# Optimization experiments

Hardware: AMD Instinct MI355X
Metric: run time of the kernel (lower is better)

Reference implementation:

```python
import jax, jax.numpy as jnp
import numpy as np
from jax import lax

T = 8192
OBS = 512
HID = 2048
NOBJ = 8


def setup_inputs() -> dict:
    key = jax.random.key(0)
    ks = jax.random.split(key, 9)
    s_in = 1.0 / np.sqrt(OBS)
    s_hid = 1.0 / np.sqrt(HID)
    return {
        "x": jax.random.normal(ks[0], (T, OBS), dtype=jnp.float32),
        "W_in": jax.random.normal(ks[1], (HID, OBS), dtype=jnp.float32) * s_in,
        "W_B": jax.random.normal(ks[2], (HID, OBS), dtype=jnp.float32) * s_in,
        "W_C": jax.random.normal(ks[3], (HID, OBS), dtype=jnp.float32) * s_in,
        "W_delta": jax.random.normal(ks[4], (HID, OBS), dtype=jnp.float32) * s_in,
        "A_log": jax.random.normal(ks[5], (HID,), dtype=jnp.float32),
        "W_out": jax.random.normal(ks[6], (NOBJ, HID), dtype=jnp.float32) * s_hid,
        "b_out": jnp.zeros((NOBJ,), dtype=jnp.float32),
        "W_skip": jax.random.normal(ks[7], (NOBJ, OBS), dtype=jnp.float32) * s_in,
    }


def reference(x, W_in, W_B, W_C, W_delta, A_log, W_out, b_out, W_skip):
    # Input-dependent SSM parameters (4 GEMMs, [T, HID] each)
    x_state = x @ W_in.T
    B = x @ W_B.T
    C = x @ W_C.T
    delta = jax.nn.sigmoid(x @ W_delta.T)
    A = -jnp.exp(A_log)                      # [HID]

    A_bar = jnp.exp(delta * A)               # [T, HID], per-step decay
    Bx = B * x_state                         # [T, HID], per-step input

    def step(h, inp):
        a, bx = inp
        h = a * h + bx
        return h, h

    h0 = jnp.zeros((HID,), dtype=x.dtype)
    _, h_seq = lax.scan(step, h0, (A_bar, Bx))  # [T, HID]

    y = C * h_seq
    out = y @ W_out.T + b_out + x @ W_skip.T    # [T, NOBJ]
    return out
```

## Files before the change

### kernel.cpp

```cpp
#include <hip/hip_runtime.h>
#include <hip/hip_bf16.h>
#include <cstdint>

#define TT   8192
#define KOBS 512
#define HID  2048
#define NOBJ 8
#define NCH  64
#define CT   128

typedef unsigned short u16;
typedef uint32_t u32;
typedef short bf16x8 __attribute__((ext_vector_type(8)));
typedef float f32x4  __attribute__((ext_vector_type(4)));
typedef unsigned short u16x4 __attribute__((ext_vector_type(4)));

static __device__ __forceinline__ float bf2f(u16 u) {
    union { uint32_t i; float f; } v;
    v.i = ((uint32_t)u) << 16;
    return v.f;
}
static __device__ __forceinline__ u16 f2bf(float f) {
    union { float f; uint32_t i; } v;
    v.f = f;
    uint32_t lsb = (v.i >> 16) & 1u;
    uint32_t r = v.i + 0x7fffu + lsb;
    return (u16)(r >> 16);
}

static __device__ __forceinline__ void async_ld16(const u16* g, u16* l) {
    __builtin_amdgcn_global_load_lds(
        (const __attribute__((address_space(1))) uint32_t*)g,
        (__attribute__((address_space(3))) uint32_t*)l,
        16, 0, 0);
}

__global__ void prep_w(const float* __restrict__ Win,
                       const float* __restrict__ WB,
                       const float* __restrict__ WC,
                       const float* __restrict__ Wd,
                       const float* __restrict__ A_log,
                       u16* __restrict__ W_bf,
                       float* __restrict__ A_e)
{
    const int tid0   = blockIdx.x * blockDim.x + threadIdx.x;
    const int stride = gridDim.x * blockDim.x;

    for (int i = tid0; i < 4 * HID * KOBS / 8; i += stride) {
        int n  = i >> 6;
        int k8 = (i & 63) * 8;
        int h  = n >> 2;
        int w  = n & 3;
        const float* src = (w == 0) ? Win : (w == 1) ? WB : (w == 2) ? WC : Wd;
        const float4* s4 = (const float4*)(src + (size_t)h * KOBS + k8);
        float4 a = s4[0], b = s4[1];
        u16x4 o1 = { f2bf(a.x), f2bf(a.y), f2bf(a.z), f2bf(a.w) };
        u16x4 o2 = { f2bf(b.x), f2bf(b.y), f2bf(b.z), f2bf(b.w) };
        *(u16x4*)&W_bf[(size_t)i * 8]     = o1;
        *(u16x4*)&W_bf[(size_t)i * 8 + 4] = o2;
    }

    if (tid0 < HID)
        A_e[tid0] = -__expf(A_log[tid0]) * 1.44269504f;
}

__launch_bounds__(256)
__global__ void prep_x_out(const float* __restrict__ x,
                           const float* __restrict__ b_out,
                           const float* __restrict__ W_skip,
                           float* __restrict__ out,
                           u16* __restrict__ x_bf)
{
    const int wave = threadIdx.x >> 6;
    const int lane = threadIdx.x & 63;
    const int t0 = (blockIdx.x * 4 + wave) * 4;

    float acc[4][NOBJ];
#pragma unroll
    for (int tt = 0; tt < 4; tt++)
#pragma unroll
        for (int o = 0; o < NOBJ; o++) acc[tt][o] = 0.f;

#pragma unroll
    for (int i = 0; i < 2; i++) {
        const int kv = (i * 64 + lane) * 4;
        float4 w[NOBJ];
#pragma unroll
        for (int o = 0; o < NOBJ; o++)
            w[o] = *(const float4*)(W_skip + (size_t)o * KOBS + kv);
#pragma unroll
        for (int tt = 0; tt < 4; tt++) {
            const size_t off = (size_t)(t0 + tt) * KOBS + kv;
            float4 xv = *(const float4*)(x + off);
            u16x4 xb = { f2bf(xv.x), f2bf(xv.y), f2bf(xv.z), f2bf(xv.w) };
            *(u16x4*)&x_bf[off] = xb;
#pragma unroll
            for (int o = 0; o < NOBJ; o++)
                acc[tt][o] += xv.x * w[o].x + xv.y * w[o].y +
                              xv.z * w[o].z + xv.w * w[o].w;
        }
    }
#pragma unroll
    for (int s = 32; s > 0; s >>= 1)
#pragma unroll
        for (int tt = 0; tt < 4; tt++)
#pragma unroll
            for (int o = 0; o < NOBJ; o++)
                acc[tt][o] += __shfl_xor(acc[tt][o], s, 64);
    if (lane == 0) {
#pragma unroll
        for (int tt = 0; tt < 4; tt++)
#pragma unroll
            for (int o = 0; o < NOBJ; o++)
                out[(size_t)(t0 + tt) * NOBJ + o] = acc[tt][o] + b_out[o];
    }
}

__launch_bounds__(256)
__global__ void gemm_fused(const u16* __restrict__ x_bf,
                           const u16* __restrict__ W_bf,
                           const float* __restrict__ A_e,
                           u16* __restrict__ YB,
                           u16* __restrict__ YC,
                           float* __restrict__ P,
                           float* __restrict__ S)
{
    __shared__ __align__(16) u16 smem[3 * 128 * 40];
    __shared__ float Ps[256], Ss[256];
    u16* a_s = smem;
    u16* b_s = smem + 4096;

    const int tid  = threadIdx.x;
    const int bm   = blockIdx.x & 63;
    const int bn   = blockIdx.x >> 6;
    const int m0t  = bm * 128;
    const int n0   = bn * 128;
    const int lane = tid & 63;
    const int wave = tid >> 6;
    const int wn   = (wave & 1) * 64;
    const int wt   = (wave >> 1) * 64;
    const int fr   = lane & 15;
    const int fq   = lane >> 4;

    f32x4 acc[4][4];
#pragma unroll
    for (int i = 0; i < 4; i++)
#pragma unroll
        for (int j = 0; j < 4; j++) {
            f32x4 z = {0.f, 0.f, 0.f, 0.f};
            acc[i][j] = z;
        }

    const int srow = tid >> 2;
    const int scg  = (tid & 3) ^ ((srow >> 1) & 3);
    const u16* gA0 = x_bf + (size_t)(m0t + srow) * KOBS + scg * 8;
    const u16* gA1 = gA0 + (size_t)64 * KOBS;
    const u16* gB0 = W_bf + (size_t)(n0 + srow) * KOBS + scg * 8;
    const u16* gB1 = gB0 + (size_t)64 * KOBS;
    u16* lA0 = &a_s[tid * 8];
    u16* lA1 = &a_s[2048 + tid * 8];
    u16* lB0 = &b_s[tid * 8];
    u16* lB1 = &b_s[2048 + tid * 8];

    const int pcg = fq ^ ((fr >> 1) & 3);

    for (int kb = 0; kb < KOBS; kb += 32) {
        async_ld16(gA0 + kb, lA0);
        async_ld16(gA1 + kb, lA1);
        async_ld16(gB0 + kb, lB0);
        async_ld16(gB1 + kb, lB1);
        __syncthreads();

        bf16x8 af[4], bfx[4];
#pragma unroll
        for (int i = 0; i < 4; i++)
            af[i] = *(const bf16x8*)&b_s[(wn + i * 16 + fr) * 32 + pcg * 8];
#pragma unroll
        for (int j = 0; j < 4; j++)
            bfx[j] = *(const bf16x8*)&a_s[(wt + j * 16 + fr) * 32 + pcg * 8];

#pragma unroll
        for (int i = 0; i < 4; i++)
#pragma unroll
            for (int j = 0; j < 4; j++)
                acc[i][j] = __builtin_amdgcn_mfma_f32_16x16x32_bf16(
                    af[i], bfx[j], acc[i][j], 0, 0, 0);
        __syncthreads();
    }

    const int hq = wn >> 2;
#pragma unroll
    for (int i = 0; i < 4; i++) {
        const int hl = hq + i * 4 + fq;
        const float ae = A_e[bn * 32 + hl];
#pragma unroll
        for (int j = 0; j < 4; j++) {
            const int tl = wt + j * 16 + fr;
            f32x4 v = acc[i][j];
            float sig = 1.0f / (1.0f + __expf(-v[3]));
            smem[(0 * 128 + tl) * 40 + hl] = f2bf(v[0] * v[1]);
            smem[(1 * 128 + tl) * 40 + hl] = f2bf(v[2]);
            smem[(2 * 128 + tl) * 40 + hl] = f2bf(sig * ae);
        }
    }
    __syncthreads();

    const int hi  = tid & 31;
    const int seg = tid >> 5;
    {
        float p = 1.f, s = 0.f;
        const int tbase = seg * 16;
#pragma unroll
        for (int t = 0; t < 16; t++) {
            float a  = exp2f(bf2f(smem[(2 * 128 + tbase + t) * 40 + hi]));
            float bx = bf2f(smem[(0 * 128 + tbase + t) * 40 + hi]);
            s = fmaf(a, s, bx);
            p *= a;
        }
        Ps[seg * 32 + hi] = p;
        Ss[seg * 32 + hi] = s;
    }
    __syncthreads();

    if (tid < 32) {
        float rr = 1.f, sr = 0.f;
#pragma unroll
        for (int sg = 0; sg < 8; sg++) {
            float ps = Ps[sg * 32 + tid], ss = Ss[sg * 32 + tid];
            Ps[sg * 32 + tid] = rr;
            Ss[sg * 32 + tid] = sr;
            sr = fmaf(ps, sr, ss);
            rr *= ps;
        }
        P[(size_t)bm * HID + bn * 32 + tid] = rr;
        S[(size_t)bm * HID + bn * 32 + tid] = sr;
    }
    __syncthreads();

    {
        const float Rp = Ps[seg * 32 + hi];
        const float Sp = Ss[seg * 32 + hi];
        float r = 1.f, s = 0.f;
        const int tbase = seg * 16;
#pragma unroll
        for (int t = 0; t < 16; t++) {
            const int row = tbase + t;
            float a  = exp2f(bf2f(smem[(2 * 128 + row) * 40 + hi]));
            float bx = bf2f(smem[(0 * 128 + row) * 40 + hi]);
            float cc = bf2f(smem[(1 * 128 + row) * 40 + hi]);
            s = fmaf(a, s, bx);
            r *= a;
            float hl = fmaf(r, Sp, s);
            smem[(0 * 128 + row) * 40 + hi] = f2bf(cc * hl);
            smem[(2 * 128 + row) * 40 + hi] = f2bf(cc * r * Rp);
        }
    }
    __syncthreads();

#pragma unroll
    for (int it = 0; it < 4; it++) {
        const int g = it * 64 + (tid >> 2);
        const int a = g >> 7;
        const int t = g & 127;
        const int c = tid & 3;
        uint4 vd = *(const uint4*)&smem[((a * 2) * 128 + t) * 40 + c * 8];
        u16* dst = (a == 0 ? YB : YC) +
                   (size_t)(m0t + t) * HID + bn * 32 + c * 8;
        *(uint4*)dst = vd;
    }
}

__global__ void scan_combine(const float* __restrict__ P,
                             const float* __restrict__ S,
                             float* __restrict__ H0)
{
    const int h = blockIdx.x * 256 + threadIdx.x;
    float hrun = 0.f;
#pragma unroll 8
    for (int c = 0; c < NCH; c++) {
        H0[c * HID + h] = hrun;
        hrun = fmaf(P[c * HID + h], hrun, S[c * HID + h]);
    }
}

__launch_bounds__(256)
__global__ void final_out(const u16* __restrict__ YB,
                          const u16* __restrict__ YC,
                          const float* __restrict__ H0,
                          const float* __restrict__ W_out,
                          float* __restrict__ out)
{
    __shared__ __align__(16) u16 ybuf[64 * 256];
    __shared__ __align__(16) u16 wst[8 * 264];
    __shared__ float h0s[256];
    const int tid  = threadIdx.x;
    const int tc   = blockIdx.x >> 3;
    const int hg   = blockIdx.x & 7;
    const int lane = tid & 63;
    const int wave = tid >> 6;
    const int fr   = lane & 15;
    const int fq   = lane >> 4;
    const int t0   = tc * 64;

#pragma unroll
    for (int o = 0; o < 8; o++)
        wst[o * 264 + tid] = f2bf(W_out[(size_t)o * HID + hg * 256 + tid]);
    h0s[tid] = H0[(size_t)(tc >> 1) * HID + hg * 256 + tid];
    __syncthreads();

    const int g   = tid & 31;
    const int tb0 = tid >> 5;
    float4 h0a = *(const float4*)&h0s[g * 8];
    float4 h0b = *(const float4*)&h0s[g * 8 + 4];
    const float h0r[8] = { h0a.x, h0a.y, h0a.z, h0a.w,
                           h0b.x, h0b.y, h0b.z, h0b.w };
#pragma unroll
    for (int k = 0; k < 8; k++) {
        const int t = tb0 + k * 8;
        const size_t off = (size_t)(t0 + t) * HID + hg * 256 + g * 8;
        bf16x8 yb = *(const bf16x8*)(YB + off);
        bf16x8 yc = *(const bf16x8*)(YC + off);
        bf16x8 yv;
#pragma unroll
        for (int e = 0; e < 8; e++) {
            float y = fmaf(bf2f((u16)yc[e]), h0r[e], bf2f((u16)yb[e]));
            yv[e] = (short)f2bf(y);
        }
        *(bf16x8*)&ybuf[t * 256 + ((g ^ (t & 7)) << 3)] = yv;
    }
    __syncthreads();

    bf16x8 bw[8];
#pragma unroll
    for (int ks = 0; ks < 8; ks++) {
        bf16x8 w = {0, 0, 0, 0, 0, 0, 0, 0};
        if (fr < 8)
            w = *(const bf16x8*)&wst[fr * 264 + ks * 32 + fq * 8];
        bw[ks] = w;
    }

    {
        const int t = wave * 16 + fr;
        f32x4 acc2 = {0.f, 0.f, 0.f, 0.f};
#pragma unroll
        for (int ks = 0; ks < 8; ks++) {
            const int gg = ks * 4 + fq;
            bf16x8 yv = *(const bf16x8*)
                &ybuf[t * 256 + ((gg ^ (fr & 7)) << 3)];
            acc2 = __builtin_amdgcn_mfma_f32_16x16x32_bf16(bw[ks], yv, acc2,
                                                           0, 0, 0);
        }
        if (fq < 2) {
            const int tg = t0 + t;
#pragma unroll
            for (int reg = 0; reg < 4; reg++)
                atomicAdd(&out[(size_t)tg * NOBJ + 4 * fq + reg], acc2[reg]);
        }
    }
}

extern "C" void kernel_launch(void* const* d_in, const int* in_sizes, int n_in,
                              void* d_out, int out_size, void* d_ws, size_t ws_size,
                              hipStream_t stream)
{
    const float* x      = (const float*)d_in[0];
    const float* Win    = (const float*)d_in[1];
    const float* WB     = (const float*)d_in[2];
    const float* WC     = (const float*)d_in[3];
    const float* Wd     = (const float*)d_in[4];
    const float* A_log  = (const float*)d_in[5];
    const float* W_out  = (const float*)d_in[6];
    const float* b_out  = (const float*)d_in[7];
    const float* W_skip = (const float*)d_in[8];
    float* out = (float*)d_out;

    char* ws = (char*)d_ws;
    size_t off = 0;
    auto alloc = [&](size_t bytes) -> void* {
        void* p = (void*)(ws + off);
        off += (bytes + 255) & ~(size_t)255;
        return p;
    };

    u16*   x_bf = (u16*)  alloc((size_t)TT * KOBS * 2);
    u16*   W_bf = (u16*)  alloc((size_t)4 * HID * KOBS * 2);
    float* A_e  = (float*)alloc((size_t)HID * 4);
    u16*   YB   = (u16*)  alloc((size_t)TT * HID * 2);
    u16*   YC   = (u16*)  alloc((size_t)TT * HID * 2);
    float* P    = (float*)alloc((size_t)NCH * HID * 4);
    float* S    = (float*)alloc((size_t)NCH * HID * 4);
    float* H0   = (float*)alloc((size_t)NCH * HID * 4);
    (void)ws_size; (void)in_sizes; (void)n_in; (void)out_size;

    prep_w<<<2048, 256, 0, stream>>>(Win, WB, WC, Wd, A_log, W_bf, A_e);
    prep_x_out<<<512, 256, 0, stream>>>(x, b_out, W_skip, out, x_bf);
    gemm_fused<<<4096, 256, 0, stream>>>(x_bf, W_bf, A_e, YB, YC, P, S);
    scan_combine<<<8, 256, 0, stream>>>(P, S, H0);
    final_out<<<1024, 256, 0, stream>>>(YB, YC, H0, W_out, out);
}
```

Measured before the change: 217.3 us.

## Fuse YB output projection into GEMM epilogue and merge prep kernels

The local-scan part of y (C times intra-chunk h) is now projected through W_out with an MFMA inside gemm_fused and atomically added to out, so the YB intermediate is never written to or read from global memory. final_out now only reads YC and folds H0 into scaled W_out weights. The two prep kernels are merged into one launch, and the second in-block scan pass is replaced by a vectorized combine using stored prefix values. The cost is many float atomics on out and bf16 rounding of intermediate prefix states.

```diff
diff --git a/kernel.cpp b/kernel.cpp
--- a/kernel.cpp
+++ b/kernel.cpp
@@ -14,6 +14,7 @@
 typedef short bf16x8 __attribute__((ext_vector_type(8)));
 typedef float f32x4  __attribute__((ext_vector_type(4)));
 typedef unsigned short u16x4 __attribute__((ext_vector_type(4)));
+typedef unsigned short u16x8 __attribute__((ext_vector_type(8)));
 
 static __device__ __forceinline__ float bf2f(u16 u) {
     union { uint32_t i; float f; } v;
@@ -35,84 +36,84 @@
         16, 0, 0);
 }
 
-__global__ void prep_w(const float* __restrict__ Win,
-                       const float* __restrict__ WB,
-                       const float* __restrict__ WC,
-                       const float* __restrict__ Wd,
-                       const float* __restrict__ A_log,
-                       u16* __restrict__ W_bf,
-                       float* __restrict__ A_e)
+__launch_bounds__(256)
+__global__ void prep_all(const float* __restrict__ x,
+                         const float* __restrict__ Win,
+                         const float* __restrict__ WB,
+                         const float* __restrict__ WC,
+                         const float* __restrict__ Wd,
+                         const float* __restrict__ A_log,
+                         const float* __restrict__ b_out,
+                         const float* __restrict__ W_skip,
+                         float* __restrict__ out,
+                         u16* __restrict__ x_bf,
+                         u16* __restrict__ W_bf,
+                         float* __restrict__ A_e)
 {
-    const int tid0   = blockIdx.x * blockDim.x + threadIdx.x;
-    const int stride = gridDim.x * blockDim.x;
-
-    for (int i = tid0; i < 4 * HID * KOBS / 8; i += stride) {
-        int n  = i >> 6;
-        int k8 = (i & 63) * 8;
-        int h  = n >> 2;
-        int w  = n & 3;
-        const float* src = (w == 0) ? Win : (w == 1) ? WB : (w == 2) ? WC : Wd;
-        const float4* s4 = (const float4*)(src + (size_t)h * KOBS + k8);
-        float4 a = s4[0], b = s4[1];
-        u16x4 o1 = { f2bf(a.x), f2bf(a.y), f2bf(a.z), f2bf(a.w) };
-        u16x4 o2 = { f2bf(b.x), f2bf(b.y), f2bf(b.z), f2bf(b.w) };
-        *(u16x4*)&W_bf[(size_t)i * 8]     = o1;
-        *(u16x4*)&W_bf[(size_t)i * 8 + 4] = o2;
-    }
-
-    if (tid0 < HID)
-        A_e[tid0] = -__expf(A_log[tid0]) * 1.44269504f;
-}
-
-__launch_bounds__(256)
-__global__ void prep_x_out(const float* __restrict__ x,
-                           const float* __restrict__ b_out,
-                           const float* __restrict__ W_skip,
-                           float* __restrict__ out,
-                           u16* __restrict__ x_bf)
-{
-    const int wave = threadIdx.x >> 6;
-    const int lane = threadIdx.x & 63;
-    const int t0 = (blockIdx.x * 4 + wave) * 4;
-
-    float acc[4][NOBJ];
-#pragma unroll
-    for (int tt = 0; tt < 4; tt++)
-#pragma unroll
-        for (int o = 0; o < NOBJ; o++) acc[tt][o] = 0.f;
-
-#pragma unroll
-    for (int i = 0; i < 2; i++) {
-        const int kv = (i * 64 + lane) * 4;
-        float4 w[NOBJ];
-#pragma unroll
-        for (int o = 0; o < NOBJ; o++)
-            w[o] = *(const float4*)(W_skip + (size_t)o * KOBS + kv);
-#pragma unroll
-        for (int tt = 0; tt < 4; tt++) {
-            const size_t off = (size_t)(t0 + tt) * KOBS + kv;
-            float4 xv = *(const float4*)(x + off);
-            u16x4 xb = { f2bf(xv.x), f2bf(xv.y), f2bf(xv.z), f2bf(xv.w) };
-            *(u16x4*)&x_bf[off] = xb;
+    if (blockIdx.x < 512) {
+        const int wave = threadIdx.x >> 6;
+        const int lane = threadIdx.x & 63;
+        const int t0 = (blockIdx.x * 4 + wave) * 4;
+
+        float acc[4][NOBJ];
+#pragma unroll
+        for (int tt = 0; tt < 4; tt++)
+#pragma unroll
+            for (int o = 0; o < NOBJ; o++) acc[tt][o] = 0.f;
+
+#pragma unroll
+        for (int i = 0; i < 2; i++) {
+            const int kv = (i * 64 + lane) * 4;
+            float4 w[NOBJ];
 #pragma unroll
             for (int o = 0; o < NOBJ; o++)
-                acc[tt][o] += xv.x * w[o].x + xv.y * w[o].y +
-                              xv.z * w[o].z + xv.w * w[o].w;
-        }
-    }
-#pragma unroll
-    for (int s = 32; s > 0; s >>= 1)
-#pragma unroll
-        for (int tt = 0; tt < 4; tt++)
-#pragma unroll
-            for (int o = 0; o < NOBJ; o++)
-                acc[tt][o] += __shfl_xor(acc[tt][o], s, 64);
-    if (lane == 0) {
-#pragma unroll
-        for (int tt = 0; tt < 4; tt++)
-#pragma unroll
-            for (int o = 0; o < NOBJ; o++)
-                out[(size_t)(t0 + tt) * NOBJ + o] = acc[tt][o] + b_out[o];
+                w[o] = *(const float4*)(W_skip + (size_t)o * KOBS + kv);
+#pragma unroll
+            for (int tt = 0; tt < 4; tt++) {
+                const size_t off = (size_t)(t0 + tt) * KOBS + kv;
+                float4 xv = *(const float4*)(x + off);
+                u16x4 xb = { f2bf(xv.x), f2bf(xv.y), f2bf(xv.z), f2bf(xv.w) };
+                *(u16x4*)&x_bf[off] = xb;
+#pragma unroll
+                for (int o = 0; o < NOBJ; o++)
+                    acc[tt][o] += xv.x * w[o].x + xv.y * w[o].y +
+                                  xv.z * w[o].z + xv.w * w[o].w;
+            }
+        }
+#pragma unroll
+        for (int s = 32; s > 0; s >>= 1)
+#pragma unroll
+            for (int tt = 0; tt < 4; tt++)
+#pragma unroll
+                for (int o = 0; o < NOBJ; o++)
+                    acc[tt][o] += __shfl_xor(acc[tt][o], s, 64);
+        if (lane == 0) {
+#pragma unroll
+            for (int tt = 0; tt < 4; tt++)
+#pragma unroll
+                for (int o = 0; o < NOBJ; o++)
+                    out[(size_t)(t0 + tt) * NOBJ + o] = acc[tt][o] + b_out[o];
+        }
+    } else {
+        const int tid0 = (blockIdx.x - 512) * 256 + threadIdx.x;
+#pragma unroll
+        for (int q = 0; q < 2; q++) {
+            const int i = tid0 + q * 262144;
+            int n  = i >> 6;
+            int k8 = (i & 63) * 8;
+            int h  = n >> 2;
+            int w  = n & 3;
+            const float* src = (w == 0) ? Win : (w == 1) ? WB
+                             : (w == 2) ? WC  : Wd;
+            const float4* s4 = (const float4*)(src + (size_t)h * KOBS + k8);
+            float4 a = s4[0], b = s4[1];
+            u16x4 o1 = { f2bf(a.x), f2bf(a.y), f2bf(a.z), f2bf(a.w) };
+            u16x4 o2 = { f2bf(b.x), f2bf(b.y), f2bf(b.z), f2bf(b.w) };
+            *(u16x4*)&W_bf[(size_t)i * 8]     = o1;
+            *(u16x4*)&W_bf[(size_t)i * 8 + 4] = o2;
+        }
+        if (tid0 < HID)
+            A_e[tid0] = -__expf(A_log[tid0]) * 1.44269504f;
     }
 }
 
@@ -120,10 +121,11 @@
 __global__ void gemm_fused(const u16* __restrict__ x_bf,
                            const u16* __restrict__ W_bf,
                            const float* __restrict__ A_e,
-                           u16* __restrict__ YB,
+                           const float* __restrict__ W_out,
                            u16* __restrict__ YC,
                            float* __restrict__ P,
-                           float* __restrict__ S)
+                           float* __restrict__ S,
+                           float* __restrict__ out)
 {
     __shared__ __align__(16) u16 smem[3 * 128 * 40];
     __shared__ float Ps[256], Ss[256];
@@ -205,17 +207,20 @@
     }
     __syncthreads();
 
-    const int hi  = tid & 31;
-    const int seg = tid >> 5;
     {
+        const int hi  = tid & 31;
+        const int seg = tid >> 5;
         float p = 1.f, s = 0.f;
         const int tbase = seg * 16;
 #pragma unroll
         for (int t = 0; t < 16; t++) {
-            float a  = exp2f(bf2f(smem[(2 * 128 + tbase + t) * 40 + hi]));
-            float bx = bf2f(smem[(0 * 128 + tbase + t) * 40 + hi]);
+            const int row = tbase + t;
+            float a  = exp2f(bf2f(smem[(2 * 128 + row) * 40 + hi]));
+            float bx = bf2f(smem[(0 * 128 + row) * 40 + hi]);
             s = fmaf(a, s, bx);
             p *= a;
+            smem[(0 * 128 + row) * 40 + hi] = f2bf(s);
+            smem[(2 * 128 + row) * 40 + hi] = f2bf(p);
         }
         Ps[seg * 32 + hi] = p;
         Ss[seg * 32 + hi] = s;
@@ -237,36 +242,61 @@
     }
     __syncthreads();
 
-    {
-        const float Rp = Ps[seg * 32 + hi];
-        const float Sp = Ss[seg * 32 + hi];
-        float r = 1.f, s = 0.f;
-        const int tbase = seg * 16;
-#pragma unroll
-        for (int t = 0; t < 16; t++) {
-            const int row = tbase + t;
-            float a  = exp2f(bf2f(smem[(2 * 128 + row) * 40 + hi]));
-            float bx = bf2f(smem[(0 * 128 + row) * 40 + hi]);
-            float cc = bf2f(smem[(1 * 128 + row) * 40 + hi]);
-            s = fmaf(a, s, bx);
-            r *= a;
-            float hl = fmaf(r, Sp, s);
-            smem[(0 * 128 + row) * 40 + hi] = f2bf(cc * hl);
-            smem[(2 * 128 + row) * 40 + hi] = f2bf(cc * r * Rp);
-        }
+#pragma unroll
+    for (int it = 0; it < 2; it++) {
+        const int idx = it * 256 + tid;
+        const int t   = idx >> 2;
+        const int cg  = idx & 3;
+        const int sg  = t >> 4;
+        u16x8 s8  = *(const u16x8*)&smem[(0 * 128 + t) * 40 + cg * 8];
+        u16x8 r8  = *(const u16x8*)&smem[(2 * 128 + t) * 40 + cg * 8];
+        u16x8 cc8 = *(const u16x8*)&smem[(1 * 128 + t) * 40 + cg * 8];
+        float4 Spa = *(const float4*)&Ss[sg * 32 + cg * 8];
+        float4 Spb = *(const float4*)&Ss[sg * 32 + cg * 8 + 4];
+        float4 Rpa = *(const float4*)&Ps[sg * 32 + cg * 8];
+        float4 Rpb = *(const float4*)&Ps[sg * 32 + cg * 8 + 4];
+        const float Sp[8] = { Spa.x, Spa.y, Spa.z, Spa.w,
+                              Spb.x, Spb.y, Spb.z, Spb.w };
+        const float Rp[8] = { Rpa.x, Rpa.y, Rpa.z, Rpa.w,
+                              Rpb.x, Rpb.y, Rpb.z, Rpb.w };
+        u16x8 yb8, yc8;
+#pragma unroll
+        for (int e = 0; e < 8; e++) {
+            float sv = bf2f(s8[e]);
+            float rv = bf2f(r8[e]);
+            float cc = bf2f(cc8[e]);
+            float hl = fmaf(rv, Sp[e], sv);
+            yb8[e] = f2bf(cc * hl);
+            yc8[e] = f2bf(cc * rv * Rp[e]);
+        }
+        *(u16x8*)(YC + (size_t)(m0t + t) * HID + bn * 32 + cg * 8) = yc8;
+        *(u16x8*)&smem[(0 * 128 + t) * 40 + cg * 8] = yb8;
     }
     __syncthreads();
 
-#pragma unroll
-    for (int it = 0; it < 4; it++) {
-        const int g = it * 64 + (tid >> 2);
-        const int a = g >> 7;
-        const int t = g & 127;
-        const int c = tid & 3;
-        uint4 vd = *(const uint4*)&smem[((a * 2) * 128 + t) * 40 + c * 8];
-        u16* dst = (a == 0 ? YB : YC) +
-                   (size_t)(m0t + t) * HID + bn * 32 + c * 8;
-        *(uint4*)dst = vd;
+    bf16x8 wfrag = {0, 0, 0, 0, 0, 0, 0, 0};
+    if (fr < 8) {
+        const float* wp = W_out + (size_t)fr * HID + bn * 32 + fq * 8;
+        float4 wa = *(const float4*)wp;
+        float4 wb = *(const float4*)(wp + 4);
+        wfrag[0] = (short)f2bf(wa.x); wfrag[1] = (short)f2bf(wa.y);
+        wfrag[2] = (short)f2bf(wa.z); wfrag[3] = (short)f2bf(wa.w);
+        wfrag[4] = (short)f2bf(wb.x); wfrag[5] = (short)f2bf(wb.y);
+        wfrag[6] = (short)f2bf(wb.z); wfrag[7] = (short)f2bf(wb.w);
+    }
+#pragma unroll
+    for (int mt = 0; mt < 2; mt++) {
+        const int tb = wave * 32 + mt * 16;
+        bf16x8 yfrag = *(const bf16x8*)&smem[(0 * 128 + tb + fr) * 40 + fq * 8];
+        f32x4 pacc = {0.f, 0.f, 0.f, 0.f};
+        pacc = __builtin_amdgcn_mfma_f32_16x16x32_bf16(wfrag, yfrag, pacc,
+                                                       0, 0, 0);
+        if (fq < 2) {
+#pragma unroll
+            for (int reg = 0; reg < 4; reg++)
+                atomicAdd(&out[(size_t)(m0t + tb + fr) * NOBJ + 4 * fq + reg],
+                          pacc[reg]);
+        }
     }
 }
 
@@ -284,15 +314,13 @@
 }
 
 __launch_bounds__(256)
-__global__ void final_out(const u16* __restrict__ YB,
-                          const u16* __restrict__ YC,
+__global__ void final_out(const u16* __restrict__ YC,
                           const float* __restrict__ H0,
                           const float* __restrict__ W_out,
                           float* __restrict__ out)
 {
     __shared__ __align__(16) u16 ybuf[64 * 256];
     __shared__ __align__(16) u16 wst[8 * 264];
-    __shared__ float h0s[256];
     const int tid  = threadIdx.x;
     const int tc   = blockIdx.x >> 3;
     const int hg   = blockIdx.x & 7;
@@ -302,30 +330,19 @@
     const int fq   = lane >> 4;
     const int t0   = tc * 64;
 
+    const float h0v = H0[(size_t)(tc >> 1) * HID + hg * 256 + tid];
 #pragma unroll
     for (int o = 0; o < 8; o++)
-        wst[o * 264 + tid] = f2bf(W_out[(size_t)o * HID + hg * 256 + tid]);
-    h0s[tid] = H0[(size_t)(tc >> 1) * HID + hg * 256 + tid];
-    __syncthreads();
+        wst[o * 264 + tid] =
+            f2bf(W_out[(size_t)o * HID + hg * 256 + tid] * h0v);
 
     const int g   = tid & 31;
     const int tb0 = tid >> 5;
-    float4 h0a = *(const float4*)&h0s[g * 8];
-    float4 h0b = *(const float4*)&h0s[g * 8 + 4];
-    const float h0r[8] = { h0a.x, h0a.y, h0a.z, h0a.w,
-                           h0b.x, h0b.y, h0b.z, h0b.w };
 #pragma unroll
     for (int k = 0; k < 8; k++) {
         const int t = tb0 + k * 8;
-        const size_t off = (size_t)(t0 + t) * HID + hg * 256 + g * 8;
-        bf16x8 yb = *(const bf16x8*)(YB + off);
-        bf16x8 yc = *(const bf16x8*)(YC + off);
-        bf16x8 yv;
-#pragma unroll
-        for (int e = 0; e < 8; e++) {
-            float y = fmaf(bf2f((u16)yc[e]), h0r[e], bf2f((u16)yb[e]));
-            yv[e] = (short)f2bf(y);
-        }
+        bf16x8 yv = *(const bf16x8*)
+            (YC + (size_t)(t0 + t) * HID + hg * 256 + g * 8);
         *(bf16x8*)&ybuf[t * 256 + ((g ^ (t & 7)) << 3)] = yv;
     }
     __syncthreads();
@@ -385,16 +402,16 @@
     u16*   x_bf = (u16*)  alloc((size_t)TT * KOBS * 2);
     u16*   W_bf = (u16*)  alloc((size_t)4 * HID * KOBS * 2);
     float* A_e  = (float*)alloc((size_t)HID * 4);
-    u16*   YB   = (u16*)  alloc((size_t)TT * HID * 2);
     u16*   YC   = (u16*)  alloc((size_t)TT * HID * 2);
     float* P    = (float*)alloc((size_t)NCH * HID * 4);
     float* S    = (float*)alloc((size_t)NCH * HID * 4);
     float* H0   = (float*)alloc((size_t)NCH * HID * 4);
     (void)ws_size; (void)in_sizes; (void)n_in; (void)out_size;
 
-    prep_w<<<2048, 256, 0, stream>>>(Win, WB, WC, Wd, A_log, W_bf, A_e);
-    prep_x_out<<<512, 256, 0, stream>>>(x, b_out, W_skip, out, x_bf);
-    gemm_fused<<<4096, 256, 0, stream>>>(x_bf, W_bf, A_e, YB, YC, P, S);
+    prep_all<<<1536, 256, 0, stream>>>(x, Win, WB, WC, Wd, A_log,
+                                       b_out, W_skip, out, x_bf, W_bf, A_e);
+    gemm_fused<<<4096, 256, 0, stream>>>(x_bf, W_bf, A_e, W_out,
+                                         YC, P, S, out);
     scan_combine<<<8, 256, 0, stream>>>(P, S, H0);
-    final_out<<<1024, 256, 0, stream>>>(YB, YC, H0, W_out, out);
-}
+    final_out<<<1024, 256, 0, stream>>>(YC, H0, W_out, out);
+}
```

Result: slower. 261.0 us (+20.1%).
